# Kernel tuning notes

Hardware: AMD Instinct MI355X
Metric: run time of the kernel (lower is better)

The kernel has to match this reference:

```python
import math
import jax, jax.numpy as jnp
import numpy as np

D_MODEL, N_HEADS, D_FF = 2048, 16, 8192
B, T = 4, 1024
D_HEAD = D_MODEL // N_HEADS
LN_EPS = 1e-5


def hadamard(x):
    """Orthonormal Hadamard transform along last dim (power-of-two length)."""
    n = x.shape[-1]
    y = x.reshape(-1, n)
    h = 1
    while h < n:
        y = y.reshape(-1, n // (2 * h), 2, h)
        a, b = y[..., 0, :], y[..., 1, :]
        y = jnp.concatenate([a + b, a - b], axis=-1).reshape(-1, n)
        h *= 2
    return (y / math.sqrt(n)).reshape(x.shape)


def quantize_int8_per_row(W):
    s = jnp.maximum(jnp.max(jnp.abs(W), axis=1, keepdims=True), 1e-8) / 127.0
    Q = jnp.clip(jnp.round(W / s), -127, 127).astype(jnp.int8)
    return Q, s


def make_dtdr_weight(key, out_f, in_f):
    W = jax.random.normal(key, (out_f, in_f), dtype=jnp.float32) * 0.02
    return quantize_int8_per_row(hadamard(W))  # W_tilde = W @ H, then int8


def setup_inputs() -> dict:
    key = jax.random.key(0)
    ks = jax.random.split(key, 8)
    x = jax.random.normal(ks[0], (B, T, D_MODEL), dtype=jnp.float32)
    Qq, sq = make_dtdr_weight(ks[1], D_MODEL, D_MODEL)
    Qk, sk = make_dtdr_weight(ks[2], D_MODEL, D_MODEL)
    Qv, sv = make_dtdr_weight(ks[3], D_MODEL, D_MODEL)
    Qo, so = make_dtdr_weight(ks[4], D_MODEL, D_MODEL)
    Qf1, sf1 = make_dtdr_weight(ks[5], D_FF, D_MODEL)
    Qf2, sf2 = make_dtdr_weight(ks[6], D_MODEL, D_FF)
    return dict(
        x=x,
        ln1_g=jnp.ones((D_MODEL,), jnp.float32), ln1_b=jnp.zeros((D_MODEL,), jnp.float32),
        ln2_g=jnp.ones((D_MODEL,), jnp.float32), ln2_b=jnp.zeros((D_MODEL,), jnp.float32),
        Qq=Qq, sq=sq, Qk=Qk, sk=sk, Qv=Qv, sv=sv, Qo=Qo, so=so,
        Qf1=Qf1, sf1=sf1, bf1=jnp.zeros((D_FF,), jnp.float32),
        Qf2=Qf2, sf2=sf2, bf2=jnp.zeros((D_MODEL,), jnp.float32),
    )


def layernorm(x, g, b):
    mu = jnp.mean(x, axis=-1, keepdims=True)
    var = jnp.mean(jnp.square(x - mu), axis=-1, keepdims=True)
    return (x - mu) / jnp.sqrt(var + LN_EPS) * g + b


def dtdr_linear(x, Q, s, bias=None):
    # y = (H x) @ dequant(Q)^T + b
    xh = hadamard(x.astype(jnp.float32))
    W = Q.astype(jnp.float32) * s  # (out, in)
    y = jnp.einsum('btd,od->bto', xh, W)
    return y if bias is None else y + bias


def reference(x, ln1_g, ln1_b, ln2_g, ln2_b, Qq, sq, Qk, sk, Qv, sv, Qo, so,
              Qf1, sf1, bf1, Qf2, sf2, bf2):
    Bc, Tc, C = x.shape
    h = layernorm(x, ln1_g, ln1_b)
    q = dtdr_linear(h, Qq, sq).reshape(Bc, Tc, N_HEADS, D_HEAD).transpose(0, 2, 1, 3)
    k = dtdr_linear(h, Qk, sk).reshape(Bc, Tc, N_HEADS, D_HEAD).transpose(0, 2, 1, 3)
    v = dtdr_linear(h, Qv, sv).reshape(Bc, Tc, N_HEADS, D_HEAD).transpose(0, 2, 1, 3)
    scores = jnp.einsum('bhqd,bhkd->bhqk', q, k) / math.sqrt(D_HEAD)
    p = jax.nn.softmax(scores, axis=-1)
    out = jnp.einsum('bhqk,bhkd->bhqd', p, v)
    out = out.transpose(0, 2, 1, 3).reshape(Bc, Tc, C)
    x = x + dtdr_linear(out, Qo, so)
    h = layernorm(x, ln2_g, ln2_b)
    ff = dtdr_linear(h, Qf1, sf1, bf1)
    ff = jax.nn.gelu(ff, approximate=False)  # torch F.gelu default = erf gelu
    x = x + dtdr_linear(ff, Qf2, sf2, bf2)
    return x
```

## Files before the change

kernel.cpp:

```cpp
#include <hip/hip_runtime.h>
#include <cstdint>
#include <cstddef>

typedef unsigned short u16;
typedef unsigned int   u32;
typedef __bf16 bf16x8 __attribute__((ext_vector_type(8)));
typedef float  f32x4  __attribute__((ext_vector_type(4)));

__device__ __forceinline__ float bf2f(u16 u) {
  union { u32 i; float f; } v; v.i = ((u32)u) << 16; return v.f;
}
__device__ __forceinline__ u16 f2bf(float f) {
  union { float f; u32 i; } v; v.f = f;
  u32 r = v.i + 0x7fffu + ((v.i >> 16) & 1u);
  return (u16)(r >> 16);
}
__device__ __forceinline__ void unpack8(uint4 raw, float* v) {
  v[0]=bf2f(raw.x&0xffff); v[1]=bf2f(raw.x>>16);
  v[2]=bf2f(raw.y&0xffff); v[3]=bf2f(raw.y>>16);
  v[4]=bf2f(raw.z&0xffff); v[5]=bf2f(raw.z>>16);
  v[6]=bf2f(raw.w&0xffff); v[7]=bf2f(raw.w>>16);
}
__device__ __forceinline__ uint4 pack8(const float* v) {
  uint4 r;
  r.x = (u32)f2bf(v[0]) | ((u32)f2bf(v[1])<<16);
  r.y = (u32)f2bf(v[2]) | ((u32)f2bf(v[3])<<16);
  r.z = (u32)f2bf(v[4]) | ((u32)f2bf(v[5])<<16);
  r.w = (u32)f2bf(v[6]) | ((u32)f2bf(v[7])<<16);
  return r;
}
__device__ __forceinline__ void gload16(const void* g, void* l) {
  __builtin_amdgcn_global_load_lds((const __attribute__((address_space(1))) void*)g,
                                   (__attribute__((address_space(3))) void*)l, 16, 0, 0);
}

template<typename T>
__device__ __forceinline__ void load8(const T* p, float* v);
template<> __device__ __forceinline__ void load8<float>(const float* p, float* v) {
  const float4 a = ((const float4*)p)[0];
  const float4 b = ((const float4*)p)[1];
  v[0]=a.x; v[1]=a.y; v[2]=a.z; v[3]=a.w;
  v[4]=b.x; v[5]=b.y; v[6]=b.z; v[7]=b.w;
}
template<> __device__ __forceinline__ void load8<u16>(const u16* p, float* v) {
  unpack8(*(const uint4*)p, v);
}

__global__ __launch_bounds__(256) void cvt_k(const int* __restrict__ Q, u16* __restrict__ W) {
  const size_t i = ((size_t)blockIdx.x * 256 + threadIdx.x) * 8;
  const int4 a = *(const int4*)(Q + i);
  const int4 b = *(const int4*)(Q + i + 4);
  union { float f; u32 u; } c;
  uint4 r;
  u32 t;
  c.f = (float)a.x; t = c.u >> 16; c.f = (float)a.y; r.x = t | (c.u & 0xffff0000u);
  c.f = (float)a.z; t = c.u >> 16; c.f = (float)a.w; r.y = t | (c.u & 0xffff0000u);
  c.f = (float)b.x; t = c.u >> 16; c.f = (float)b.y; r.z = t | (c.u & 0xffff0000u);
  c.f = (float)b.z; t = c.u >> 16; c.f = (float)b.w; r.w = t | (c.u & 0xffff0000u);
  *(uint4*)(W + i) = r;
}

__global__ __launch_bounds__(256) void scat_k(const float* __restrict__ a,
    const float* __restrict__ b, const float* __restrict__ c, float* __restrict__ o) {
  const int i = blockIdx.x * 256 + threadIdx.x;
  o[i] = (i < 2048) ? a[i] : (i < 4096 ? b[i - 2048] : c[i - 4096]);
}

template<typename T>
__global__ __launch_bounds__(256) void ln_fwht_k(const T* __restrict__ X,
    const float* __restrict__ G, const float* __restrict__ Bt, u16* __restrict__ O) {
  __shared__ float buf[2048];
  __shared__ float red[8];
  const int tid = threadIdx.x;
  const int lane = tid & 63, wave = tid >> 6;
  const size_t base = (size_t)blockIdx.x * 2048;
  float v[8]; load8(X + base + tid*8, v);
  float s = 0.f, s2 = 0.f;
  for (int j = 0; j < 8; ++j) { s += v[j]; s2 += v[j]*v[j]; }
  for (int m = 1; m < 64; m <<= 1) { s += __shfl_xor(s, m, 64); s2 += __shfl_xor(s2, m, 64); }
  if (lane == 0) { red[wave] = s; red[4 + wave] = s2; }
  __syncthreads();
  s  = red[0] + red[1] + red[2] + red[3];
  s2 = red[4] + red[5] + red[6] + red[7];
  const float mu = s * (1.f/2048.f);
  const float rstd = rsqrtf(s2 * (1.f/2048.f) - mu*mu + 1e-5f);
  float g[8], bb[8];
  load8(G + tid*8, g); load8(Bt + tid*8, bb);
  for (int j = 0; j < 8; ++j) buf[tid*8 + j] = (v[j] - mu) * rstd * g[j] + bb[j];
  __syncthreads();
  for (int h = 1; h < 2048; h <<= 1) {
    for (int p = 0; p < 4; ++p) {
      const int idx = p*256 + tid;
      const int i = ((idx & ~(h-1)) << 1) | (idx & (h-1));
      const float a = buf[i], c = buf[i + h];
      buf[i] = a + c; buf[i + h] = a - c;
    }
    __syncthreads();
  }
  float o[8];
  for (int j = 0; j < 8; ++j) o[j] = buf[tid*8 + j] * 0.02209708691207961f;
  *(uint4*)&O[base + tid*8] = pack8(o);
}

template<int N>
__global__ __launch_bounds__(256) void fwht_ip(u16* __restrict__ D) {
  __shared__ float buf[N];
  const int tid = threadIdx.x;
  const size_t base = (size_t)blockIdx.x * N;
  constexpr int V8 = N / (8*256);
  for (int i = 0; i < V8; ++i) {
    uint4 raw = *(const uint4*)&D[base + (i*256 + tid)*8];
    float v[8]; unpack8(raw, v);
    for (int j = 0; j < 8; ++j) buf[(i*256 + tid)*8 + j] = v[j];
  }
  __syncthreads();
  constexpr int PAIRS = N / 2 / 256;
  for (int h = 1; h < N; h <<= 1) {
    for (int p = 0; p < PAIRS; ++p) {
      const int idx = p*256 + tid;
      const int i = ((idx & ~(h-1)) << 1) | (idx & (h-1));
      const float a = buf[i], c = buf[i + h];
      buf[i] = a + c; buf[i + h] = a - c;
    }
    __syncthreads();
  }
  const float sc = rsqrtf((float)N);
  for (int i = 0; i < V8; ++i) {
    float v[8];
    for (int j = 0; j < 8; ++j) v[j] = buf[(i*256 + tid)*8 + j] * sc;
    *(uint4*)&D[base + (i*256 + tid)*8] = pack8(v);
  }
}

__global__ __launch_bounds__(512, 1) void gemm256(
    const u16* __restrict__ A, const u16* __restrict__ Bw, const float* __restrict__ S,
    void* __restrict__ C, int ldc, int M, int N, int K,
    const float* __restrict__ bias, const float* __restrict__ resf,
    const u16* __restrict__ resb, int dogelu, int outf32)
{
  __shared__ alignas(16) u16 sA[3][256*64];
  __shared__ alignas(16) u16 sB[3][128*64];
  const int tid = threadIdx.x;
  const int lane = tid & 63, wave = tid >> 6;
  const int quad = lane >> 4, l16 = lane & 15;
  const int wm = wave & 3, wn = wave >> 2;
  const int nwg = gridDim.x * gridDim.y;
  int flat = blockIdx.y * gridDim.x + blockIdx.x;
  if ((nwg & 7) == 0) flat = (flat & 7) * (nwg >> 3) + (flat >> 3);
  const long tM = (long)(flat % gridDim.x) * 256;
  const long tN = (long)(flat / gridDim.x) * 128;

  const int rc = lane >> 3;
  const int cswz = ((lane & 7) ^ rc) * 8;
  const u16* Ab = A  + (size_t)(tM + rc) * K + cswz;
  const u16* Bb = Bw + (size_t)(tN + rc) * K + cswz;

  auto stage = [&](int buf, int k0) {
#pragma unroll
    for (int i = 0; i < 4; ++i) {
      const int chunk = i*8 + wave;
      gload16(Ab + (size_t)(chunk*8)*K + k0, &sA[buf][chunk*512]);
    }
#pragma unroll
    for (int i = 0; i < 2; ++i) {
      const int chunk = i*8 + wave;
      gload16(Bb + (size_t)(chunk*8)*K + k0, &sB[buf][chunk*512]);
    }
  };

  f32x4 acc[4][4] = {};
  auto compute = [&](int buf) {
#pragma unroll
    for (int ks = 0; ks < 2; ++ks) {
      bf16x8 af[4], bq[4];
      const int oc = ks*4 + quad;
#pragma unroll
      for (int mt = 0; mt < 4; ++mt)
        af[mt] = *(const bf16x8*)&sA[buf][(wm*64 + mt*16 + l16)*64 + ((oc ^ (l16 & 7)))*8];
#pragma unroll
      for (int nt = 0; nt < 4; ++nt)
        bq[nt] = *(const bf16x8*)&sB[buf][(wn*64 + nt*16 + l16)*64 + ((oc ^ (l16 & 7)))*8];
      __builtin_amdgcn_s_setprio(1);
#pragma unroll
      for (int mt = 0; mt < 4; ++mt)
#pragma unroll
        for (int nt = 0; nt < 4; ++nt)
          acc[mt][nt] = __builtin_amdgcn_mfma_f32_16x16x32_bf16(af[mt], bq[nt], acc[mt][nt], 0, 0, 0);
      __builtin_amdgcn_s_setprio(0);
    }
  };

  const int ntk = K >> 6;
  stage(0, 0);
  if (ntk > 1) stage(1, 64);
  for (int t = 0; t < ntk; ++t) {
    if (t + 1 < ntk) { asm volatile("s_waitcnt vmcnt(6)" ::: "memory"); }
    else             { asm volatile("s_waitcnt vmcnt(0)" ::: "memory"); }
    __builtin_amdgcn_s_barrier();
    __builtin_amdgcn_sched_barrier(0);
    if (t + 2 < ntk) stage((t + 2) % 3, (t + 2) << 6);
    compute(t % 3);
  }

#pragma unroll
  for (int in = 0; in < 4; ++in) {
    const long col = tN + wn*64 + in*16 + l16;
    const float sc = S[col];
    const float bv = bias ? bias[col] : 0.f;
#pragma unroll
    for (int im = 0; im < 4; ++im) {
      const long row0 = tM + wm*64 + im*16 + quad*4;
#pragma unroll
      for (int r = 0; r < 4; ++r) {
        float v = acc[im][in][r] * sc + bv;
        if (dogelu) v = 0.5f * v * (1.f + erff(v * 0.7071067811865475f));
        const size_t off = (size_t)(row0 + r)*ldc + col;
        if (resf) v += resf[off];
        if (resb) v += bf2f(resb[off]);
        if (outf32) ((float*)C)[off] = v;
        else        ((u16*)C)[off]   = f2bf(v);
      }
    }
  }
}

__global__ __launch_bounds__(256, 2) void attn_k(const u16* __restrict__ QKV, u16* __restrict__ O)
{
  __shared__ alignas(16) u16 sKV[16384];
  __shared__ alignas(16) u16 sP[16384];
  const int tid = threadIdx.x;
  const int lane = tid & 63, wave = tid >> 6;
  const int quad = lane >> 4, l16 = lane & 15;
  const int qt = blockIdx.x;
  const int bh = blockIdx.y;
  const int b = bh >> 4, h = bh & 15;
  const size_t rb = (size_t)b * 1024;
  const u16* Qg = QKV + (rb + (size_t)qt*128)*6144 + h*128;
  const u16* Kg = QKV + rb*6144 + 2048 + h*128;
  const u16* Vg = QKV + rb*6144 + 4096 + h*128;

  for (int c = 0; c < 8; ++c) {
    const int chunk = c*4 + wave;
    const int r = chunk*4 + quad;
    gload16(Qg + (size_t)r*6144 + l16*8, &sP[chunk*512]);
  }
  __syncthreads();
  bf16x8 aq[2][4];
  for (int im = 0; im < 2; ++im)
    for (int kk = 0; kk < 4; ++kk)
      aq[im][kk] = *(const bf16x8*)&sP[(wave*32 + im*16 + l16)*128 + kk*32 + quad*8];

  float mrun[2][4], lrun[2][4];
  f32x4 oacc[2][8] = {};
  for (int im = 0; im < 2; ++im)
    for (int r = 0; r < 4; ++r) { mrun[im][r] = -1e30f; lrun[im][r] = 0.f; }

  for (int kt = 0; kt < 8; ++kt) {
    __syncthreads();
    for (int c = 0; c < 8; ++c) {
      const int chunk = c*4 + wave;
      const int r = chunk*4 + quad;
      gload16(Kg + (size_t)(kt*128 + r)*6144 + l16*8, &sKV[chunk*512]);
    }
    __syncthreads();
    f32x4 sf[2][8] = {};
#pragma unroll
    for (int kk = 0; kk < 4; ++kk)
#pragma unroll
      for (int jn = 0; jn < 8; ++jn) {
        const bf16x8 bk = *(const bf16x8*)&sKV[(jn*16 + l16)*128 + kk*32 + quad*8];
        sf[0][jn] = __builtin_amdgcn_mfma_f32_16x16x32_bf16(aq[0][kk], bk, sf[0][jn], 0, 0, 0);
        sf[1][jn] = __builtin_amdgcn_mfma_f32_16x16x32_bf16(aq[1][kk], bk, sf[1][jn], 0, 0, 0);
      }
    const float scale = 0.08838834764831845f;
#pragma unroll
    for (int im = 0; im < 2; ++im)
#pragma unroll
      for (int r = 0; r < 4; ++r) {
        float mx = -1e30f;
        for (int jn = 0; jn < 8; ++jn) mx = fmaxf(mx, sf[im][jn][r] * scale);
        for (int m = 1; m < 16; m <<= 1) mx = fmaxf(mx, __shfl_xor(mx, m, 64));
        const float mold = mrun[im][r];
        const float mnew = fmaxf(mold, mx);
        const float alpha = __expf(mold - mnew);
        float ls = 0.f;
        for (int jn = 0; jn < 8; ++jn) {
          const float p = __expf(sf[im][jn][r] * scale - mnew);
          ls += p;
          sP[wave*4096 + (im*16 + quad*4 + r)*128 + jn*16 + l16] = f2bf(p);
        }
        for (int m = 1; m < 16; m <<= 1) ls += __shfl_xor(ls, m, 64);
        lrun[im][r] = lrun[im][r]*alpha + ls;
        mrun[im][r] = mnew;
        for (int od = 0; od < 8; ++od) oacc[im][od][r] *= alpha;
      }
    __syncthreads();
    for (int c = 0; c < 8; ++c) {
      const int chunk = c*256 + tid;
      const int kv = chunk >> 4;
      const int db = (chunk & 15) * 8;
      const uint4 raw = *(const uint4*)(Vg + (size_t)(kt*128 + kv)*6144 + db);
      const u32 w0[4] = {raw.x, raw.y, raw.z, raw.w};
      for (int j = 0; j < 4; ++j) {
        sKV[(db + 2*j  )*128 + kv] = (u16)(w0[j] & 0xffff);
        sKV[(db + 2*j+1)*128 + kv] = (u16)(w0[j] >> 16);
      }
    }
    __syncthreads();
#pragma unroll
    for (int kk = 0; kk < 4; ++kk) {
      const bf16x8 ap0 = *(const bf16x8*)&sP[wave*4096 + (     l16)*128 + kk*32 + quad*8];
      const bf16x8 ap1 = *(const bf16x8*)&sP[wave*4096 + (16 + l16)*128 + kk*32 + quad*8];
#pragma unroll
      for (int od = 0; od < 8; ++od) {
        const bf16x8 bv = *(const bf16x8*)&sKV[(od*16 + l16)*128 + kk*32 + quad*8];
        oacc[0][od] = __builtin_amdgcn_mfma_f32_16x16x32_bf16(ap0, bv, oacc[0][od], 0, 0, 0);
        oacc[1][od] = __builtin_amdgcn_mfma_f32_16x16x32_bf16(ap1, bv, oacc[1][od], 0, 0, 0);
      }
    }
  }
  for (int im = 0; im < 2; ++im)
    for (int r = 0; r < 4; ++r) {
      const float inv = 1.f / lrun[im][r];
      const size_t row = rb + (size_t)qt*128 + wave*32 + im*16 + quad*4 + r;
      for (int od = 0; od < 8; ++od)
        O[row*2048 + h*128 + od*16 + l16] = f2bf(oacc[im][od][r] * inv);
    }
}

extern "C" void kernel_launch(void* const* d_in, const int* in_sizes, int n_in,
                              void* d_out, int out_size, void* d_ws, size_t ws_size,
                              hipStream_t stream) {
  const float* x    = (const float*)d_in[0];
  const float* ln1g = (const float*)d_in[1];
  const float* ln1b = (const float*)d_in[2];
  const float* ln2g = (const float*)d_in[3];
  const float* ln2b = (const float*)d_in[4];
  const int* Qq  = (const int*)d_in[5];  const float* sq  = (const float*)d_in[6];
  const int* Qk  = (const int*)d_in[7];  const float* sk  = (const float*)d_in[8];
  const int* Qv  = (const int*)d_in[9];  const float* sv  = (const float*)d_in[10];
  const int* Qo  = (const int*)d_in[11]; const float* so  = (const float*)d_in[12];
  const int* Qf1 = (const int*)d_in[13]; const float* sf1 = (const float*)d_in[14];
  const float* bf1 = (const float*)d_in[15];
  const int* Qf2 = (const int*)d_in[16]; const float* sf2 = (const float*)d_in[17];
  const float* bf2 = (const float*)d_in[18];

  u16* XH   = (u16*)d_ws;
  u16* Wq   = XH + 8388608;
  u16* Wsl  = XH + 8388608;
  u16* QKVb = XH + 20971520;
  u16* FFb  = XH + 16777216;
  u16* Wf2  = XH;
  float* Scat = (float*)(XH + 46137344);
  float* Xout = (float*)d_out;
  if (ws_size < (size_t)100663296) return;

  ln_fwht_k<float><<<4096, 256, 0, stream>>>(x, ln1g, ln1b, XH);

  cvt_k<<<2048, 256, 0, stream>>>(Qq, Wq);
  cvt_k<<<2048, 256, 0, stream>>>(Qk, Wq + 4194304);
  cvt_k<<<2048, 256, 0, stream>>>(Qv, Wq + 8388608);
  scat_k<<<24, 256, 0, stream>>>(sq, sk, sv, Scat);
  gemm256<<<dim3(16,48), 512, 0, stream>>>(XH, Wq, Scat, QKVb, 6144, 4096, 6144, 2048,
                                           nullptr, nullptr, nullptr, 0, 0);

  attn_k<<<dim3(8, 64), 256, 0, stream>>>(QKVb, XH);

  fwht_ip<2048><<<4096, 256, 0, stream>>>(XH);

  cvt_k<<<2048, 256, 0, stream>>>(Qo, Wsl);
  gemm256<<<dim3(16,16), 512, 0, stream>>>(XH, Wsl, so, Xout, 2048, 4096, 2048, 2048,
                                           nullptr, x, nullptr, 0, 1);

  ln_fwht_k<float><<<4096, 256, 0, stream>>>(Xout, ln2g, ln2b, XH);

  cvt_k<<<4096, 256, 0, stream>>>(Qf1, Wsl);
  gemm256<<<dim3(16,32), 512, 0, stream>>>(XH, Wsl, sf1,        FFb + 0,    8192, 4096, 4096, 2048,
                                           bf1,        nullptr, nullptr, 1, 0);
  cvt_k<<<4096, 256, 0, stream>>>(Qf1 + (size_t)4096*2048, Wsl);
  gemm256<<<dim3(16,32), 512, 0, stream>>>(XH, Wsl, sf1 + 4096, FFb + 4096, 8192, 4096, 4096, 2048,
                                           bf1 + 4096, nullptr, nullptr, 1, 0);

  fwht_ip<8192><<<4096, 256, 0, stream>>>(FFb);

  cvt_k<<<8192, 256, 0, stream>>>(Qf2, Wf2);
  gemm256<<<dim3(16,16), 512, 0, stream>>>(FFb, Wf2, sf2, Xout, 2048, 4096, 2048, 8192,
                                           bf2, Xout, nullptr, 0, 1);
}
```

Before: 1.203 ms.

## Swizzle attention LDS layouts, prefetch V early, interleave GEMM staging with MFMA

```diff
diff --git a/kernel.cpp b/kernel.cpp
--- a/kernel.cpp
+++ b/kernel.cpp
@@ -33,6 +33,7 @@
   __builtin_amdgcn_global_load_lds((const __attribute__((address_space(1))) void*)g,
                                    (__attribute__((address_space(3))) void*)l, 16, 0, 0);
 }
+__device__ __forceinline__ int swz8(int row) { return ((row >> 3) ^ row) & 7; }
 
 template<typename T>
 __device__ __forceinline__ void load8(const T* p, float* v);
@@ -155,31 +156,52 @@
   const u16* Ab = A  + (size_t)(tM + rc) * K + cswz;
   const u16* Bb = Bw + (size_t)(tN + rc) * K + cswz;
 
-  auto stage = [&](int buf, int k0) {
-#pragma unroll
-    for (int i = 0; i < 4; ++i) {
-      const int chunk = i*8 + wave;
-      gload16(Ab + (size_t)(chunk*8)*K + k0, &sA[buf][chunk*512]);
-    }
-#pragma unroll
-    for (int i = 0; i < 2; ++i) {
-      const int chunk = i*8 + wave;
-      gload16(Bb + (size_t)(chunk*8)*K + k0, &sB[buf][chunk*512]);
-    }
+  f32x4 acc[4][4] = {};
+  const int ntk = K >> 6;
+
+  auto stageA = [&](int buf, int k0, int i) {
+    const int chunk = i*8 + wave;
+    gload16(Ab + (size_t)(chunk*8)*K + k0, &sA[buf][chunk*512]);
   };
-
-  f32x4 acc[4][4] = {};
-  auto compute = [&](int buf) {
+  auto stageB = [&](int buf, int k0, int i) {
+    const int chunk = i*8 + wave;
+    gload16(Bb + (size_t)(chunk*8)*K + k0, &sB[buf][chunk*512]);
+  };
+
+  stageA(0, 0, 0); stageA(0, 0, 1); stageA(0, 0, 2); stageA(0, 0, 3);
+  stageB(0, 0, 0); stageB(0, 0, 1);
+  if (ntk > 1) {
+    stageA(1, 64, 0); stageA(1, 64, 1); stageA(1, 64, 2); stageA(1, 64, 3);
+    stageB(1, 64, 0); stageB(1, 64, 1);
+  }
+  asm volatile("s_waitcnt vmcnt(6)" ::: "memory");
+  __builtin_amdgcn_s_barrier();
+  __builtin_amdgcn_sched_barrier(0);
+
+  for (int t = 0; t < ntk; ++t) {
+    const int buf = t % 3, nb = (t + 2) % 3;
+    const bool more = (t + 2) < ntk;
+    const int k2 = (t + 2) << 6;
+    bf16x8 af[4], bq[4];
 #pragma unroll
     for (int ks = 0; ks < 2; ++ks) {
-      bf16x8 af[4], bq[4];
       const int oc = ks*4 + quad;
 #pragma unroll
       for (int mt = 0; mt < 4; ++mt)
-        af[mt] = *(const bf16x8*)&sA[buf][(wm*64 + mt*16 + l16)*64 + ((oc ^ (l16 & 7)))*8];
+        af[mt] = *(const bf16x8*)&sA[buf][(wm*64 + mt*16 + l16)*64 + (oc ^ (l16 & 7))*8];
 #pragma unroll
       for (int nt = 0; nt < 4; ++nt)
-        bq[nt] = *(const bf16x8*)&sB[buf][(wn*64 + nt*16 + l16)*64 + ((oc ^ (l16 & 7)))*8];
+        bq[nt] = *(const bf16x8*)&sB[buf][(wn*64 + nt*16 + l16)*64 + (oc ^ (l16 & 7))*8];
+      if (more) {
+        if (ks == 0) { stageA(nb, k2, 0); stageA(nb, k2, 1); stageB(nb, k2, 0); }
+        else         { stageA(nb, k2, 2); stageA(nb, k2, 3); stageB(nb, k2, 1); }
+      }
+      if (ks == 1 && t + 1 < ntk) {
+        if (more) asm volatile("s_waitcnt vmcnt(6)" ::: "memory");
+        else      asm volatile("s_waitcnt vmcnt(0)" ::: "memory");
+      }
+      __builtin_amdgcn_s_barrier();
+      __builtin_amdgcn_sched_barrier(0);
       __builtin_amdgcn_s_setprio(1);
 #pragma unroll
       for (int mt = 0; mt < 4; ++mt)
@@ -187,19 +209,9 @@
         for (int nt = 0; nt < 4; ++nt)
           acc[mt][nt] = __builtin_amdgcn_mfma_f32_16x16x32_bf16(af[mt], bq[nt], acc[mt][nt], 0, 0, 0);
       __builtin_amdgcn_s_setprio(0);
-    }
-  };
-
-  const int ntk = K >> 6;
-  stage(0, 0);
-  if (ntk > 1) stage(1, 64);
-  for (int t = 0; t < ntk; ++t) {
-    if (t + 1 < ntk) { asm volatile("s_waitcnt vmcnt(6)" ::: "memory"); }
-    else             { asm volatile("s_waitcnt vmcnt(0)" ::: "memory"); }
-    __builtin_amdgcn_s_barrier();
-    __builtin_amdgcn_sched_barrier(0);
-    if (t + 2 < ntk) stage((t + 2) % 3, (t + 2) << 6);
-    compute(t % 3);
+      __builtin_amdgcn_s_barrier();
+      __builtin_amdgcn_sched_barrier(0);
+    }
   }
 
 #pragma unroll
@@ -242,13 +254,15 @@
   for (int c = 0; c < 8; ++c) {
     const int chunk = c*4 + wave;
     const int r = chunk*4 + quad;
-    gload16(Qg + (size_t)r*6144 + l16*8, &sP[chunk*512]);
+    gload16(Qg + (size_t)r*6144 + (l16 ^ swz8(r))*8, &sP[chunk*512]);
   }
   __syncthreads();
   bf16x8 aq[2][4];
   for (int im = 0; im < 2; ++im)
-    for (int kk = 0; kk < 4; ++kk)
-      aq[im][kk] = *(const bf16x8*)&sP[(wave*32 + im*16 + l16)*128 + kk*32 + quad*8];
+    for (int kk = 0; kk < 4; ++kk) {
+      const int row = wave*32 + im*16 + l16;
+      aq[im][kk] = *(const bf16x8*)&sP[row*128 + ((kk*4 + quad) ^ swz8(row))*8];
+    }
 
   float mrun[2][4], lrun[2][4];
   f32x4 oacc[2][8] = {};
@@ -260,7 +274,16 @@
     for (int c = 0; c < 8; ++c) {
       const int chunk = c*4 + wave;
       const int r = chunk*4 + quad;
-      gload16(Kg + (size_t)(kt*128 + r)*6144 + l16*8, &sKV[chunk*512]);
+      gload16(Kg + (size_t)(kt*128 + r)*6144 + (l16 ^ swz8(r))*8, &sKV[chunk*512]);
+    }
+    uint4 va[4], vb[4];
+#pragma unroll
+    for (int c = 0; c < 4; ++c) {
+      const int task = c*256 + tid;
+      const int kv = (task >> 4) * 2;
+      const int d0 = (task & 15) * 8;
+      va[c] = *(const uint4*)(Vg + (size_t)(kt*128 + kv    )*6144 + d0);
+      vb[c] = *(const uint4*)(Vg + (size_t)(kt*128 + kv + 1)*6144 + d0);
     }
     __syncthreads();
     f32x4 sf[2][8] = {};
@@ -268,7 +291,8 @@
     for (int kk = 0; kk < 4; ++kk)
 #pragma unroll
       for (int jn = 0; jn < 8; ++jn) {
-        const bf16x8 bk = *(const bf16x8*)&sKV[(jn*16 + l16)*128 + kk*32 + quad*8];
+        const int rk = jn*16 + l16;
+        const bf16x8 bk = *(const bf16x8*)&sKV[rk*128 + ((kk*4 + quad) ^ swz8(rk))*8];
         sf[0][jn] = __builtin_amdgcn_mfma_f32_16x16x32_bf16(aq[0][kk], bk, sf[0][jn], 0, 0, 0);
         sf[1][jn] = __builtin_amdgcn_mfma_f32_16x16x32_bf16(aq[1][kk], bk, sf[1][jn], 0, 0, 0);
       }
@@ -284,10 +308,11 @@
         const float mnew = fmaxf(mold, mx);
         const float alpha = __expf(mold - mnew);
         float ls = 0.f;
+        const int rl = im*16 + quad*4 + r;
         for (int jn = 0; jn < 8; ++jn) {
           const float p = __expf(sf[im][jn][r] * scale - mnew);
           ls += p;
-          sP[wave*4096 + (im*16 + quad*4 + r)*128 + jn*16 + l16] = f2bf(p);
+          sP[wave*4096 + rl*128 + (((jn*2 + (l16 >> 3)) ^ swz8(rl))*8 | (l16 & 7))] = f2bf(p);
         }
         for (int m = 1; m < 16; m <<= 1) ls += __shfl_xor(ls, m, 64);
         lrun[im][r] = lrun[im][r]*alpha + ls;
@@ -295,25 +320,31 @@
         for (int od = 0; od < 8; ++od) oacc[im][od][r] *= alpha;
       }
     __syncthreads();
-    for (int c = 0; c < 8; ++c) {
-      const int chunk = c*256 + tid;
-      const int kv = chunk >> 4;
-      const int db = (chunk & 15) * 8;
-      const uint4 raw = *(const uint4*)(Vg + (size_t)(kt*128 + kv)*6144 + db);
-      const u32 w0[4] = {raw.x, raw.y, raw.z, raw.w};
-      for (int j = 0; j < 4; ++j) {
-        sKV[(db + 2*j  )*128 + kv] = (u16)(w0[j] & 0xffff);
-        sKV[(db + 2*j+1)*128 + kv] = (u16)(w0[j] >> 16);
+#pragma unroll
+    for (int c = 0; c < 4; ++c) {
+      const int task = c*256 + tid;
+      const int kv = (task >> 4) * 2;
+      const int d0 = (task & 15) * 8;
+      const int cc = kv >> 3;
+      const u16* pa = (const u16*)&va[c];
+      const u16* pb = (const u16*)&vb[c];
+#pragma unroll
+      for (int j = 0; j < 8; ++j) {
+        const int row = d0 + j;
+        const int col = ((cc ^ swz8(row))*8) | (kv & 7);
+        *(u32*)&sKV[row*128 + col] = (u32)pa[j] | ((u32)pb[j] << 16);
       }
     }
     __syncthreads();
 #pragma unroll
     for (int kk = 0; kk < 4; ++kk) {
-      const bf16x8 ap0 = *(const bf16x8*)&sP[wave*4096 + (     l16)*128 + kk*32 + quad*8];
-      const bf16x8 ap1 = *(const bf16x8*)&sP[wave*4096 + (16 + l16)*128 + kk*32 + quad*8];
+      const int r0 = l16, r1 = 16 + l16;
+      const bf16x8 ap0 = *(const bf16x8*)&sP[wave*4096 + r0*128 + ((kk*4 + quad) ^ swz8(r0))*8];
+      const bf16x8 ap1 = *(const bf16x8*)&sP[wave*4096 + r1*128 + ((kk*4 + quad) ^ swz8(r1))*8];
 #pragma unroll
       for (int od = 0; od < 8; ++od) {
-        const bf16x8 bv = *(const bf16x8*)&sKV[(od*16 + l16)*128 + kk*32 + quad*8];
+        const int rv = od*16 + l16;
+        const bf16x8 bv = *(const bf16x8*)&sKV[rv*128 + ((kk*4 + quad) ^ swz8(rv))*8];
         oacc[0][od] = __builtin_amdgcn_mfma_f32_16x16x32_bf16(ap0, bv, oacc[0][od], 0, 0, 0);
         oacc[1][od] = __builtin_amdgcn_mfma_f32_16x16x32_bf16(ap1, bv, oacc[1][od], 0, 0, 0);
       }
```

Result: slower. 1.295 ms (+7.7%).

## Interleave global-to-LDS loads with MFMA sub-steps in bf16 GEMM mainloop

Applied to the files above, without the earlier changes.

```diff
diff --git a/kernel.cpp b/kernel.cpp
--- a/kernel.cpp
+++ b/kernel.cpp
@@ -155,31 +155,52 @@
   const u16* Ab = A  + (size_t)(tM + rc) * K + cswz;
   const u16* Bb = Bw + (size_t)(tN + rc) * K + cswz;
 
-  auto stage = [&](int buf, int k0) {
-#pragma unroll
-    for (int i = 0; i < 4; ++i) {
-      const int chunk = i*8 + wave;
-      gload16(Ab + (size_t)(chunk*8)*K + k0, &sA[buf][chunk*512]);
-    }
-#pragma unroll
-    for (int i = 0; i < 2; ++i) {
-      const int chunk = i*8 + wave;
-      gload16(Bb + (size_t)(chunk*8)*K + k0, &sB[buf][chunk*512]);
-    }
+  f32x4 acc[4][4] = {};
+  const int ntk = K >> 6;
+
+  auto stageA = [&](int buf, int k0, int i) {
+    const int chunk = i*8 + wave;
+    gload16(Ab + (size_t)(chunk*8)*K + k0, &sA[buf][chunk*512]);
   };
-
-  f32x4 acc[4][4] = {};
-  auto compute = [&](int buf) {
+  auto stageB = [&](int buf, int k0, int i) {
+    const int chunk = i*8 + wave;
+    gload16(Bb + (size_t)(chunk*8)*K + k0, &sB[buf][chunk*512]);
+  };
+
+  stageA(0, 0, 0); stageA(0, 0, 1); stageA(0, 0, 2); stageA(0, 0, 3);
+  stageB(0, 0, 0); stageB(0, 0, 1);
+  if (ntk > 1) {
+    stageA(1, 64, 0); stageA(1, 64, 1); stageA(1, 64, 2); stageA(1, 64, 3);
+    stageB(1, 64, 0); stageB(1, 64, 1);
+  }
+  asm volatile("s_waitcnt vmcnt(6)" ::: "memory");
+  __builtin_amdgcn_s_barrier();
+  __builtin_amdgcn_sched_barrier(0);
+
+  for (int t = 0; t < ntk; ++t) {
+    const int buf = t % 3, nb = (t + 2) % 3;
+    const bool more = (t + 2) < ntk;
+    const int k2 = (t + 2) << 6;
+    bf16x8 af[4], bq[4];
 #pragma unroll
     for (int ks = 0; ks < 2; ++ks) {
-      bf16x8 af[4], bq[4];
       const int oc = ks*4 + quad;
 #pragma unroll
       for (int mt = 0; mt < 4; ++mt)
-        af[mt] = *(const bf16x8*)&sA[buf][(wm*64 + mt*16 + l16)*64 + ((oc ^ (l16 & 7)))*8];
+        af[mt] = *(const bf16x8*)&sA[buf][(wm*64 + mt*16 + l16)*64 + (oc ^ (l16 & 7))*8];
 #pragma unroll
       for (int nt = 0; nt < 4; ++nt)
-        bq[nt] = *(const bf16x8*)&sB[buf][(wn*64 + nt*16 + l16)*64 + ((oc ^ (l16 & 7)))*8];
+        bq[nt] = *(const bf16x8*)&sB[buf][(wn*64 + nt*16 + l16)*64 + (oc ^ (l16 & 7))*8];
+      if (more) {
+        if (ks == 0) { stageA(nb, k2, 0); stageA(nb, k2, 1); stageB(nb, k2, 0); }
+        else         { stageA(nb, k2, 2); stageA(nb, k2, 3); stageB(nb, k2, 1); }
+      }
+      if (ks == 1 && t + 1 < ntk) {
+        if (more) asm volatile("s_waitcnt vmcnt(6)" ::: "memory");
+        else      asm volatile("s_waitcnt vmcnt(0)" ::: "memory");
+      }
+      __builtin_amdgcn_s_barrier();
+      __builtin_amdgcn_sched_barrier(0);
       __builtin_amdgcn_s_setprio(1);
 #pragma unroll
       for (int mt = 0; mt < 4; ++mt)
@@ -187,19 +208,9 @@
         for (int nt = 0; nt < 4; ++nt)
           acc[mt][nt] = __builtin_amdgcn_mfma_f32_16x16x32_bf16(af[mt], bq[nt], acc[mt][nt], 0, 0, 0);
       __builtin_amdgcn_s_setprio(0);
-    }
-  };
-
-  const int ntk = K >> 6;
-  stage(0, 0);
-  if (ntk > 1) stage(1, 64);
-  for (int t = 0; t < ntk; ++t) {
-    if (t + 1 < ntk) { asm volatile("s_waitcnt vmcnt(6)" ::: "memory"); }
-    else             { asm volatile("s_waitcnt vmcnt(0)" ::: "memory"); }
-    __builtin_amdgcn_s_barrier();
-    __builtin_amdgcn_sched_barrier(0);
-    if (t + 2 < ntk) stage((t + 2) % 3, (t + 2) << 6);
-    compute(t % 3);
+      __builtin_amdgcn_s_barrier();
+      __builtin_amdgcn_sched_barrier(0);
+    }
   }
 
 #pragma unroll
```

Measured after the change: 1.100 ms. 1.09x faster.
